# Kernel tuning notes

Hardware: AMD Instinct MI355X
Metric: run time of the kernel (lower is better)

## Reference

```python
import jax, jax.numpy as jnp
import numpy as np

N_NODES = 10000
N_EDGES = 640000
IN_DIM = 128
HID = 128
N_GRAPHS = 64


def setup_inputs() -> dict:
    key = jax.random.key(0)
    ks = jax.random.split(key, 9)
    x = jax.random.normal(ks[0], (N_NODES, IN_DIM), dtype=jnp.float32)
    edge_index = jax.random.randint(ks[1], (2, N_EDGES), 0, N_NODES, dtype=jnp.int32)
    batch = jnp.sort(jax.random.randint(ks[2], (N_NODES,), 0, N_GRAPHS, dtype=jnp.int32))
    # GCNConv weights (glorot-ish init) and zero biases
    W0 = jax.random.normal(ks[3], (IN_DIM, HID), dtype=jnp.float32) / np.float32(np.sqrt(IN_DIM))
    b0 = jnp.zeros((HID,), dtype=jnp.float32)
    W1 = jax.random.normal(ks[4], (HID, HID), dtype=jnp.float32) / np.float32(np.sqrt(HID))
    b1 = jnp.zeros((HID,), dtype=jnp.float32)
    W2 = jax.random.normal(ks[5], (HID, HID), dtype=jnp.float32) / np.float32(np.sqrt(HID))
    b2 = jnp.zeros((HID,), dtype=jnp.float32)
    return {"x": x, "edge_index": edge_index, "batch": batch,
            "W0": W0, "b0": b0, "W1": W1, "b1": b1, "W2": W2, "b2": b2}


def _gcn_conv(x, src, dst, W, b, n_nodes):
    """PyG GCNConv: self-loops + symmetric normalization, then linear+bias."""
    h = x @ W  # [N, H]
    # degree of destination nodes, +1 for the added self-loop
    deg = jax.ops.segment_sum(jnp.ones((src.shape[0],), h.dtype), dst,
                              num_segments=n_nodes) + 1.0
    dis = jax.lax.rsqrt(deg)  # deg >= 1 so no inf guard needed
    # messages along real edges, normalized by dis[src]*dis[dst]
    msg = h[src] * (dis[src] * dis[dst])[:, None]  # [E, H]
    out = jax.ops.segment_sum(msg, dst, num_segments=n_nodes)
    # self-loop contribution: dis[i]^2 * h[i]
    out = out + h * (dis * dis)[:, None]
    return out + b


def reference(x, edge_index, batch, W0, b0, W1, b1, W2, b2):
    src, dst = edge_index[0], edge_index[1]
    n_nodes = x.shape[0]
    # layer 0 and 1 followed by ReLU (dropout: eval mode -> identity)
    h = _gcn_conv(x, src, dst, W0, b0, n_nodes)
    h = jax.nn.relu(h)
    h = _gcn_conv(h, src, dst, W1, b1, n_nodes)
    h = jax.nn.relu(h)
    h = _gcn_conv(h, src, dst, W2, b2, n_nodes)
    # global mean pool over batch indices
    sums = jax.ops.segment_sum(h, batch, num_segments=N_GRAPHS)  # [B, H]
    counts = jax.ops.segment_sum(jnp.ones((n_nodes,), h.dtype), batch,
                                 num_segments=N_GRAPHS)
    return sums / jnp.maximum(counts, 1.0)[:, None]
```

## Files before the change

kernel.cpp:

```cpp
#include <hip/hip_runtime.h>
#include <hip/hip_fp16.h>

#define NN 10000
#define NE 640000
#define NG 64
#define CAP 128
#define NB 625
#define BCAP 1280

typedef _Float16 f16x8 __attribute__((ext_vector_type(8)));
typedef float f32x4 __attribute__((ext_vector_type(4)));

__device__ __forceinline__ void split8v(float4 xa, float4 xb, f16x8& ah, f16x8& al) {
    float x[8] = {xa.x, xa.y, xa.z, xa.w, xb.x, xb.y, xb.z, xb.w};
#pragma unroll
    for (int j = 0; j < 8; j++) {
        ah[j] = (_Float16)x[j];
        al[j] = (_Float16)(x[j] - (float)ah[j]);
    }
}

__global__ __launch_bounds__(256) void k_initp1(
    const int* __restrict__ batch, int* __restrict__ gstart,
    const float* __restrict__ W0, const float* __restrict__ W1, const float* __restrict__ W2,
    __half* __restrict__ wh, __half* __restrict__ wl,
    const int* __restrict__ ei, int* __restrict__ bcur, int* __restrict__ pk,
    __half* __restrict__ g16a, __half* __restrict__ g16b)
{
    __shared__ int hist[NB];
    int bid = blockIdx.x, t = threadIdx.x;
    if (bid < 40) {
        int i = bid * 256 + t;
        if (i < NN) {
            int b = batch[i];
            int prev = (i == 0) ? -1 : batch[i - 1];
            for (int g = prev + 1; g <= b; g++) gstart[g] = i;
            if (i == NN - 1)
                for (int g = b + 1; g <= NG; g++) gstart[g] = NN;
        }
    } else if (bid < 232) {
        int wid = bid - 40;
        int z = wid >> 6;
        int q = (wid & 63) * 256 + t;
        int c = q >> 7, k = q & 127;
        const float* W = (z == 0) ? W0 : (z == 1) ? W1 : W2;
        float v = W[k * 128 + c];
        __half h = __float2half(v);
        __half lo = __float2half(v - __half2float(h));
        wh[z * 16384 + c * 128 + k] = h;
        wl[z * 16384 + c * 128 + k] = lo;
    } else if (bid < 389) {
        for (int q = t; q < NB; q += 256) hist[q] = 0;
        __syncthreads();
        int4 s4[4], d4[4];
        int ebase = (bid - 232) * 4096;
#pragma unroll
        for (int q = 0; q < 4; q++) {
            int e = ebase + q * 1024 + t * 4;
            if (e < NE) {
                s4[q] = *(const int4*)&ei[e];
                d4[q] = *(const int4*)&ei[NE + e];
                atomicAdd(&hist[d4[q].x >> 4], 1);
                atomicAdd(&hist[d4[q].y >> 4], 1);
                atomicAdd(&hist[d4[q].z >> 4], 1);
                atomicAdd(&hist[d4[q].w >> 4], 1);
            }
        }
        __syncthreads();
        for (int q = t; q < NB; q += 256) {
            int h = hist[q];
            hist[q] = (h > 0) ? atomicAdd(&bcur[q], h) : 0;
        }
        __syncthreads();
#pragma unroll
        for (int q = 0; q < 4; q++) {
            int e = ebase + q * 1024 + t * 4;
            if (e < NE) {
                int b0i = d4[q].x >> 4, b1i = d4[q].y >> 4, b2i = d4[q].z >> 4, b3i = d4[q].w >> 4;
                int r0 = atomicAdd(&hist[b0i], 1);
                int r1 = atomicAdd(&hist[b1i], 1);
                int r2 = atomicAdd(&hist[b2i], 1);
                int r3 = atomicAdd(&hist[b3i], 1);
                if (r0 < BCAP) pk[b0i * BCAP + r0] = s4[q].x | ((d4[q].x & 15) << 14);
                if (r1 < BCAP) pk[b1i * BCAP + r1] = s4[q].y | ((d4[q].y & 15) << 14);
                if (r2 < BCAP) pk[b2i * BCAP + r2] = s4[q].z | ((d4[q].z & 15) << 14);
                if (r3 < BCAP) pk[b3i * BCAP + r3] = s4[q].w | ((d4[q].w & 15) << 14);
            }
        }
    } else {
        uint4 z = {0u, 0u, 0u, 0u};
        ((uint4*)(g16a + NN * 128))[t] = z;
        ((uint4*)(g16b + NN * 128))[t] = z;
    }
}

__global__ __launch_bounds__(512) void k_p2g0(
    const int* __restrict__ bcur, const int* __restrict__ pk,
    const float* __restrict__ x,
    const __half* __restrict__ whT, const __half* __restrict__ wlT,
    int* __restrict__ deg, int* __restrict__ csrc, __half* __restrict__ g16a)
{
    __shared__ int buf[16 * CAP];
    __shared__ int cnt[16];
    int b = blockIdx.x, t = threadIdx.x;
    if (t < 16) cnt[t] = 0;
    __syncthreads();

    int n = bcur[b];
    if (n > BCAP) n = BCAP;
    const int* pb = &pk[b * BCAP];
    for (int i = t; i < n; i += 512) {
        int v = pb[i];
        int nd = v >> 14;
        int slot = atomicAdd(&cnt[nd], 1);
        if (slot < CAP) buf[(nd << 7) + slot] = v & 0x3FFF;
    }
    __syncthreads();

    int node0 = b << 4;
    if (t < 16) {
        int c = cnt[t];
        deg[node0 + t] = c;
        buf[(t << 7) + min(c, CAP - 1)] = NN;
    }
    __syncthreads();

    ((int4*)&csrc[node0 << 7])[t] = ((const int4*)buf)[t];

    int w = t >> 6, l = t & 63, lr = l & 15, lg = l >> 4;
    int cw = w * 16;
    const _Float16* whp = (const _Float16*)whT;
    const _Float16* wlp = (const _Float16*)wlT;
    f32x4 acc = {0.f, 0.f, 0.f, 0.f};
#pragma unroll
    for (int ks = 0; ks < 4; ks++) {
        int kb = ks * 32 + lg * 8;
        f16x8 ah, al;
        split8v(*(const float4*)&x[(node0 + lr) * 128 + kb],
                *(const float4*)&x[(node0 + lr) * 128 + kb + 4], ah, al);
        int c0 = cw + lr;
        f16x8 bh = *(const f16x8*)&whp[c0 * 128 + kb];
        f16x8 bl = *(const f16x8*)&wlp[c0 * 128 + kb];
        acc = __builtin_amdgcn_mfma_f32_16x16x32_f16(ah, bh, acc, 0, 0, 0);
        acc = __builtin_amdgcn_mfma_f32_16x16x32_f16(al, bh, acc, 0, 0, 0);
        acc = __builtin_amdgcn_mfma_f32_16x16x32_f16(ah, bl, acc, 0, 0, 0);
    }
#pragma unroll
    for (int reg = 0; reg < 4; reg++) {
        int row = lg * 4 + reg;
        float d = rsqrtf((float)cnt[row] + 1.0f);
        g16a[(node0 + row) * 128 + cw + lr] = __float2half(acc[reg] * d);
    }
}

__device__ __forceinline__ void accp(uint2 v, float2& p, float2& q) {
    float2 f0 = __half22float2(*(__half2*)&v.x);
    float2 f1 = __half22float2(*(__half2*)&v.y);
    p.x += f0.x; p.y += f0.y; q.x += f1.x; q.y += f1.y;
}

__global__ __launch_bounds__(512) void k_ag(
    const __half* __restrict__ gin, const float* __restrict__ bias,
    const int* __restrict__ deg, const int* __restrict__ csrc,
    const __half* __restrict__ whT, const __half* __restrict__ wlT,
    __half* __restrict__ gout)
{
    __shared__ float Xs[16][132];
    int base = blockIdx.x << 4;
    int t = threadIdx.x;
    int w = t >> 6, l = t & 63;
    int half = l >> 5, li = l & 31;
    int co = li * 4;
#pragma unroll
    for (int k4 = 0; k4 < 2; k4++) {
        int row = w * 2 + k4;
        int i = base + row;
        int dgi = __builtin_amdgcn_readfirstlane(deg[i]);
        int nn_ = min(dgi, CAP - 1);
        int np = (nn_ + 1) & ~1;
        float2 A0 = {0.f, 0.f}, A1 = {0.f, 0.f};
        float2 B0 = {0.f, 0.f}, B1 = {0.f, 0.f};
        if (half == 0) {
            uint2 sv = *(const uint2*)&gin[i * 128 + co];
            A0 = __half22float2(*(__half2*)&sv.x);
            A1 = __half22float2(*(__half2*)&sv.y);
        }
        const int* cp = &csrc[i << 7];
        for (int bs = 0; bs < np; bs += 64) {
            int m = np - bs;
            if (m > 64) m = 64;
            int myedge = (l < m) ? cp[bs + l] : NN;
            int pairs = m >> 1;
            int j = 0;
            for (; j + 8 <= pairs; j += 8) {
                int r0 = __shfl(myedge, 2 * j + half);
                int r1 = __shfl(myedge, 2 * j + 2 + half);
                int r2 = __shfl(myedge, 2 * j + 4 + half);
                int r3 = __shfl(myedge, 2 * j + 6 + half);
                int r4 = __shfl(myedge, 2 * j + 8 + half);
                int r5 = __shfl(myedge, 2 * j + 10 + half);
                int r6 = __shfl(myedge, 2 * j + 12 + half);
                int r7 = __shfl(myedge, 2 * j + 14 + half);
                uint2 v0 = *(const uint2*)&gin[r0 * 128 + co];
                uint2 v1 = *(const uint2*)&gin[r1 * 128 + co];
                uint2 v2 = *(const uint2*)&gin[r2 * 128 + co];
                uint2 v3 = *(const uint2*)&gin[r3 * 128 + co];
                uint2 v4 = *(const uint2*)&gin[r4 * 128 + co];
                uint2 v5 = *(const uint2*)&gin[r5 * 128 + co];
                uint2 v6 = *(const uint2*)&gin[r6 * 128 + co];
                uint2 v7 = *(const uint2*)&gin[r7 * 128 + co];
                accp(v0, A0, A1); accp(v1, B0, B1);
                accp(v2, A0, A1); accp(v3, B0, B1);
                accp(v4, A0, A1); accp(v5, B0, B1);
                accp(v6, A0, A1); accp(v7, B0, B1);
            }
            for (; j < pairs; j++) {
                int r = __shfl(myedge, 2 * j + half);
                uint2 v = *(const uint2*)&gin[r * 128 + co];
                accp(v, A0, A1);
            }
        }
        A0.x += B0.x; A0.y += B0.y; A1.x += B1.x; A1.y += B1.y;
        A0.x += __shfl_xor(A0.x, 32);
        A0.y += __shfl_xor(A0.y, 32);
        A1.x += __shfl_xor(A1.x, 32);
        A1.y += __shfl_xor(A1.y, 32);
        if (half == 0) {
            float di = rsqrtf((float)dgi + 1.0f);
            float4 bb = *(const float4*)&bias[co];
            float4 o;
            o.x = fmaxf(di * A0.x + bb.x, 0.f);
            o.y = fmaxf(di * A0.y + bb.y, 0.f);
            o.z = fmaxf(di * A1.x + bb.z, 0.f);
            o.w = fmaxf(di * A1.y + bb.w, 0.f);
            *(float4*)&Xs[row][co] = o;
        }
    }
    __syncthreads();

    int lr = l & 15, lg = l >> 4;
    int cw = w * 16;
    const _Float16* whp = (const _Float16*)whT;
    const _Float16* wlp = (const _Float16*)wlT;
    f32x4 acc = {0.f, 0.f, 0.f, 0.f};
#pragma unroll
    for (int ks = 0; ks < 4; ks++) {
        int kb = ks * 32 + lg * 8;
        f16x8 ah, al;
        split8v(*(const float4*)&Xs[lr][kb], *(const float4*)&Xs[lr][kb + 4], ah, al);
        int c0 = cw + lr;
        f16x8 bh = *(const f16x8*)&whp[c0 * 128 + kb];
        f16x8 bl = *(const f16x8*)&wlp[c0 * 128 + kb];
        acc = __builtin_amdgcn_mfma_f32_16x16x32_f16(ah, bh, acc, 0, 0, 0);
        acc = __builtin_amdgcn_mfma_f32_16x16x32_f16(al, bh, acc, 0, 0, 0);
        acc = __builtin_amdgcn_mfma_f32_16x16x32_f16(ah, bl, acc, 0, 0, 0);
    }
#pragma unroll
    for (int reg = 0; reg < 4; reg++) {
        int row = lg * 4 + reg;
        float d = rsqrtf((float)deg[base + row] + 1.0f);
        gout[(base + row) * 128 + cw + lr] = __float2half(acc[reg] * d);
    }
}

__global__ __launch_bounds__(256) void k_agg(const __half* __restrict__ g16,
                                             const float* __restrict__ bias,
                                             const int* __restrict__ deg,
                                             const int* __restrict__ csrc,
                                             float* __restrict__ out) {
    int wid = blockIdx.x * 4 + (threadIdx.x >> 6);
    int l = threadIdx.x & 63;
    if (wid >= NN) return;
    int i = wid;
    int dgi = __builtin_amdgcn_readfirstlane(deg[i]);
    int n = min(dgi, CAP - 1);
    int np = (n + 1) & ~1;
    int half = l >> 5, li = l & 31;
    int co = li * 4;
    float2 A0 = {0.f, 0.f}, A1 = {0.f, 0.f};
    float2 B0 = {0.f, 0.f}, B1 = {0.f, 0.f};
    if (half == 0) {
        uint2 sv = *(const uint2*)&g16[i * 128 + co];
        A0 = __half22float2(*(__half2*)&sv.x);
        A1 = __half22float2(*(__half2*)&sv.y);
    }
    const int* cp = &csrc[i << 7];
    for (int base = 0; base < np; base += 64) {
        int m = np - base;
        if (m > 64) m = 64;
        int myedge = (l < m) ? cp[base + l] : NN;
        int pairs = m >> 1;
        int j = 0;
        for (; j + 8 <= pairs; j += 8) {
            int r0 = __shfl(myedge, 2 * j + half);
            int r1 = __shfl(myedge, 2 * j + 2 + half);
            int r2 = __shfl(myedge, 2 * j + 4 + half);
            int r3 = __shfl(myedge, 2 * j + 6 + half);
            int r4 = __shfl(myedge, 2 * j + 8 + half);
            int r5 = __shfl(myedge, 2 * j + 10 + half);
            int r6 = __shfl(myedge, 2 * j + 12 + half);
            int r7 = __shfl(myedge, 2 * j + 14 + half);
            uint2 v0 = *(const uint2*)&g16[r0 * 128 + co];
            uint2 v1 = *(const uint2*)&g16[r1 * 128 + co];
            uint2 v2 = *(const uint2*)&g16[r2 * 128 + co];
            uint2 v3 = *(const uint2*)&g16[r3 * 128 + co];
            uint2 v4 = *(const uint2*)&g16[r4 * 128 + co];
            uint2 v5 = *(const uint2*)&g16[r5 * 128 + co];
            uint2 v6 = *(const uint2*)&g16[r6 * 128 + co];
            uint2 v7 = *(const uint2*)&g16[r7 * 128 + co];
            accp(v0, A0, A1); accp(v1, B0, B1);
            accp(v2, A0, A1); accp(v3, B0, B1);
            accp(v4, A0, A1); accp(v5, B0, B1);
            accp(v6, A0, A1); accp(v7, B0, B1);
        }
        for (; j < pairs; j++) {
            int r = __shfl(myedge, 2 * j + half);
            uint2 v = *(const uint2*)&g16[r * 128 + co];
            accp(v, A0, A1);
        }
    }
    A0.x += B0.x; A0.y += B0.y; A1.x += B1.x; A1.y += B1.y;
    A0.x += __shfl_xor(A0.x, 32);
    A0.y += __shfl_xor(A0.y, 32);
    A1.x += __shfl_xor(A1.x, 32);
    A1.y += __shfl_xor(A1.y, 32);
    if (half == 0) {
        float di = rsqrtf((float)dgi + 1.0f);
        float4 bb = *(const float4*)&bias[co];
        float4 o;
        o.x = di * A0.x + bb.x;
        o.y = di * A0.y + bb.y;
        o.z = di * A1.x + bb.z;
        o.w = di * A1.y + bb.w;
        *(float4*)&out[i * 128 + co] = o;
    }
}

__global__ __launch_bounds__(256) void k_pool(const float* __restrict__ h,
                                              const int* __restrict__ gstart,
                                              float* __restrict__ out) {
    int g = blockIdx.x;
    int s = gstart[g], e = gstart[g + 1];
    int t = threadIdx.x;
    int c = t & 127, half = t >> 7;
    float acc = 0.f;
    for (int n = s + half; n < e; n += 2) acc += h[n * 128 + c];
    __shared__ float sm[256];
    sm[t] = acc;
    __syncthreads();
    if (half == 0) {
        float cnt = (float)max(e - s, 1);
        out[g * 128 + c] = (sm[c] + sm[128 + c]) / cnt;
    }
}

extern "C" void kernel_launch(void* const* d_in, const int* in_sizes, int n_in,
                              void* d_out, int out_size, void* d_ws, size_t ws_size,
                              hipStream_t stream) {
    const float* x     = (const float*)d_in[0];
    const int*   ei    = (const int*)d_in[1];
    const int*   batch = (const int*)d_in[2];
    const float* W0 = (const float*)d_in[3];
    const float* b0 = (const float*)d_in[4];
    const float* W1 = (const float*)d_in[5];
    const float* b1 = (const float*)d_in[6];
    const float* W2 = (const float*)d_in[7];
    const float* b2 = (const float*)d_in[8];
    float* out = (float*)d_out;

    float* ws    = (float*)d_ws;
    int*   deg   = (int*)ws;
    int*   gstart= (int*)(ws + 10240);
    int*   bcur  = (int*)(ws + 10320);
    int*   csrc  = (int*)(ws + 10960);
    __half* g16a = (__half*)(ws + 1290960);
    __half* g16b = (__half*)(ws + 1931984);
    float* abuf  = ws + 2573008;
    int*   pk    = (int*)(ws + 2573008);
    __half* wh   = (__half*)(ws + 3853008);
    __half* wlo  = (__half*)(ws + 3877584);

    hipMemsetAsync(bcur, 0, 640 * sizeof(int), stream);
    k_initp1<<<390, 256, 0, stream>>>(batch, gstart, W0, W1, W2, wh, wlo, ei, bcur, pk,
                                      g16a, g16b);
    k_p2g0<<<NB, 512, 0, stream>>>(bcur, pk, x, wh, wlo, deg, csrc, g16a);
    k_ag<<<NB, 512, 0, stream>>>(g16a, b0, deg, csrc, wh + 16384, wlo + 16384, g16b);
    k_ag<<<NB, 512, 0, stream>>>(g16b, b1, deg, csrc, wh + 32768, wlo + 32768, g16a);
    k_agg<<<2500, 256, 0, stream>>>(g16a, b2, deg, csrc, abuf);
    k_pool<<<NG, 256, 0, stream>>>(abuf, gstart, out);
}
```

Baseline: 184.7 us.

## Fuse final aggregation with mean pooling via atomics and last-block finalize

Merges the last GCN aggregation kernel with the global mean pool. Each node's output row is atomically added into per-graph sums, and the last block to finish (tracked by a ticket counter) divides by the node counts and writes the result. This drops a kernel launch and the write and re-read of the full node feature buffer. In exchange it adds many float atomics to 64 contended graph rows, a threadfence per block, and order-dependent float sums. The workspace layout is also reshuffled to zero the counters and sums in a single memset.

```diff
diff --git a/kernel.cpp b/kernel.cpp
--- a/kernel.cpp
+++ b/kernel.cpp
@@ -263,14 +263,17 @@
     }
 }
 
-__global__ __launch_bounds__(256) void k_agg(const __half* __restrict__ g16,
-                                             const float* __restrict__ bias,
-                                             const int* __restrict__ deg,
-                                             const int* __restrict__ csrc,
-                                             float* __restrict__ out) {
+__global__ __launch_bounds__(256) void k_aggpool(const __half* __restrict__ g16,
+                                                 const float* __restrict__ bias,
+                                                 const int* __restrict__ deg,
+                                                 const int* __restrict__ csrc,
+                                                 const int* __restrict__ batch,
+                                                 const int* __restrict__ gstart,
+                                                 float* __restrict__ psum,
+                                                 int* __restrict__ done,
+                                                 float* __restrict__ out) {
     int wid = blockIdx.x * 4 + (threadIdx.x >> 6);
     int l = threadIdx.x & 63;
-    if (wid >= NN) return;
     int i = wid;
     int dgi = __builtin_amdgcn_readfirstlane(deg[i]);
     int n = min(dgi, CAP - 1);
@@ -327,30 +330,27 @@
     if (half == 0) {
         float di = rsqrtf((float)dgi + 1.0f);
         float4 bb = *(const float4*)&bias[co];
-        float4 o;
-        o.x = di * A0.x + bb.x;
-        o.y = di * A0.y + bb.y;
-        o.z = di * A1.x + bb.z;
-        o.w = di * A1.y + bb.w;
-        *(float4*)&out[i * 128 + co] = o;
-    }
-}
-
-__global__ __launch_bounds__(256) void k_pool(const float* __restrict__ h,
-                                              const int* __restrict__ gstart,
-                                              float* __restrict__ out) {
-    int g = blockIdx.x;
-    int s = gstart[g], e = gstart[g + 1];
-    int t = threadIdx.x;
-    int c = t & 127, half = t >> 7;
-    float acc = 0.f;
-    for (int n = s + half; n < e; n += 2) acc += h[n * 128 + c];
-    __shared__ float sm[256];
-    sm[t] = acc;
-    __syncthreads();
-    if (half == 0) {
-        float cnt = (float)max(e - s, 1);
-        out[g * 128 + c] = (sm[c] + sm[128 + c]) / cnt;
+        int g = batch[i];
+        float* ps = &psum[g * 128 + co];
+        atomicAdd(&ps[0], di * A0.x + bb.x);
+        atomicAdd(&ps[1], di * A0.y + bb.y);
+        atomicAdd(&ps[2], di * A1.x + bb.z);
+        atomicAdd(&ps[3], di * A1.y + bb.w);
+    }
+    __threadfence();
+    __syncthreads();
+    __shared__ int ticket;
+    if (threadIdx.x == 0) ticket = atomicAdd(done, 1);
+    __syncthreads();
+    if (ticket == 2499) {
+        __threadfence();
+        int t = threadIdx.x;
+        for (int q = t; q < NG * 128; q += 256) {
+            int g = q >> 7;
+            float cnt = (float)max(gstart[g + 1] - gstart[g], 1);
+            float v = __hip_atomic_load(&psum[q], __ATOMIC_RELAXED, __HIP_MEMORY_SCOPE_AGENT);
+            out[q] = v / cnt;
+        }
     }
 }
 
@@ -372,20 +372,20 @@
     int*   deg   = (int*)ws;
     int*   gstart= (int*)(ws + 10240);
     int*   bcur  = (int*)(ws + 10320);
-    int*   csrc  = (int*)(ws + 10960);
-    __half* g16a = (__half*)(ws + 1290960);
-    __half* g16b = (__half*)(ws + 1931984);
-    float* abuf  = ws + 2573008;
-    int*   pk    = (int*)(ws + 2573008);
-    __half* wh   = (__half*)(ws + 3853008);
-    __half* wlo  = (__half*)(ws + 3877584);
-
-    hipMemsetAsync(bcur, 0, 640 * sizeof(int), stream);
+    int*   done  = (int*)(ws + 10960);
+    float* psum  = ws + 10976;
+    int*   csrc  = (int*)(ws + 19168);
+    __half* g16a = (__half*)(ws + 1299168);
+    __half* g16b = (__half*)(ws + 1940192);
+    int*   pk    = (int*)(ws + 2581216);
+    __half* wh   = (__half*)(ws + 3381216);
+    __half* wlo  = (__half*)(ws + 3405792);
+
+    hipMemsetAsync(ws + 10320, 0, (640 + 16 + 8192) * sizeof(int), stream);
     k_initp1<<<390, 256, 0, stream>>>(batch, gstart, W0, W1, W2, wh, wlo, ei, bcur, pk,
                                       g16a, g16b);
     k_p2g0<<<NB, 512, 0, stream>>>(bcur, pk, x, wh, wlo, deg, csrc, g16a);
     k_ag<<<NB, 512, 0, stream>>>(g16a, b0, deg, csrc, wh + 16384, wlo + 16384, g16b);
     k_ag<<<NB, 512, 0, stream>>>(g16b, b1, deg, csrc, wh + 32768, wlo + 32768, g16a);
-    k_agg<<<2500, 256, 0, stream>>>(g16a, b2, deg, csrc, abuf);
-    k_pool<<<NG, 256, 0, stream>>>(abuf, gstart, out);
-}
+    k_aggpool<<<2500, 256, 0, stream>>>(g16a, b2, deg, csrc, batch, gstart, psum, done, out);
+}
```

After: 332.6 us. 1.8x slower.

## Fuse final aggregation with mean pooling via atomic adds into output

Applied to the files above, without the earlier changes.

The last-layer aggregation now scales each node's result by its graph's inverse count and atomically adds it into the pooled output, removing the intermediate [N,128] float buffer and the separate pool kernel. The output is pre-initialized with bias (or zero for empty graphs) by block 0 of an earlier kernel. This saves one launch and a full write/read of the node features, but adds many float atomics contending on only 64 graph rows, and the summation order becomes nondeterministic.

```diff
diff --git a/kernel.cpp b/kernel.cpp
--- a/kernel.cpp
+++ b/kernel.cpp
@@ -98,11 +98,19 @@
     const int* __restrict__ bcur, const int* __restrict__ pk,
     const float* __restrict__ x,
     const __half* __restrict__ whT, const __half* __restrict__ wlT,
-    int* __restrict__ deg, int* __restrict__ csrc, __half* __restrict__ g16a)
+    const float* __restrict__ b2, const int* __restrict__ gstart,
+    int* __restrict__ deg, int* __restrict__ csrc, __half* __restrict__ g16a,
+    float* __restrict__ out)
 {
     __shared__ int buf[16 * CAP];
     __shared__ int cnt[16];
     int b = blockIdx.x, t = threadIdx.x;
+    if (b == 0) {
+        for (int q = t; q < NG * 128; q += 512) {
+            int g = q >> 7;
+            out[q] = (gstart[g + 1] > gstart[g]) ? b2[q & 127] : 0.f;
+        }
+    }
     if (t < 16) cnt[t] = 0;
     __syncthreads();
 
@@ -263,14 +271,14 @@
     }
 }
 
-__global__ __launch_bounds__(256) void k_agg(const __half* __restrict__ g16,
-                                             const float* __restrict__ bias,
-                                             const int* __restrict__ deg,
-                                             const int* __restrict__ csrc,
-                                             float* __restrict__ out) {
+__global__ __launch_bounds__(256) void k_aggpool(const __half* __restrict__ g16,
+                                                 const int* __restrict__ deg,
+                                                 const int* __restrict__ csrc,
+                                                 const int* __restrict__ batch,
+                                                 const int* __restrict__ gstart,
+                                                 float* __restrict__ out) {
     int wid = blockIdx.x * 4 + (threadIdx.x >> 6);
     int l = threadIdx.x & 63;
-    if (wid >= NN) return;
     int i = wid;
     int dgi = __builtin_amdgcn_readfirstlane(deg[i]);
     int n = min(dgi, CAP - 1);
@@ -326,31 +334,14 @@
     A1.y += __shfl_xor(A1.y, 32);
     if (half == 0) {
         float di = rsqrtf((float)dgi + 1.0f);
-        float4 bb = *(const float4*)&bias[co];
-        float4 o;
-        o.x = di * A0.x + bb.x;
-        o.y = di * A0.y + bb.y;
-        o.z = di * A1.x + bb.z;
-        o.w = di * A1.y + bb.w;
-        *(float4*)&out[i * 128 + co] = o;
-    }
-}
-
-__global__ __launch_bounds__(256) void k_pool(const float* __restrict__ h,
-                                              const int* __restrict__ gstart,
-                                              float* __restrict__ out) {
-    int g = blockIdx.x;
-    int s = gstart[g], e = gstart[g + 1];
-    int t = threadIdx.x;
-    int c = t & 127, half = t >> 7;
-    float acc = 0.f;
-    for (int n = s + half; n < e; n += 2) acc += h[n * 128 + c];
-    __shared__ float sm[256];
-    sm[t] = acc;
-    __syncthreads();
-    if (half == 0) {
-        float cnt = (float)max(e - s, 1);
-        out[g * 128 + c] = (sm[c] + sm[128 + c]) / cnt;
+        int g = batch[i];
+        float icnt = 1.0f / (float)max(gstart[g + 1] - gstart[g], 1);
+        float s = di * icnt;
+        float* op = &out[g * 128 + co];
+        atomicAdd(&op[0], s * A0.x);
+        atomicAdd(&op[1], s * A0.y);
+        atomicAdd(&op[2], s * A1.x);
+        atomicAdd(&op[3], s * A1.y);
     }
 }
 
@@ -375,17 +366,15 @@
     int*   csrc  = (int*)(ws + 10960);
     __half* g16a = (__half*)(ws + 1290960);
     __half* g16b = (__half*)(ws + 1931984);
-    float* abuf  = ws + 2573008;
     int*   pk    = (int*)(ws + 2573008);
-    __half* wh   = (__half*)(ws + 3853008);
-    __half* wlo  = (__half*)(ws + 3877584);
+    __half* wh   = (__half*)(ws + 3373008);
+    __half* wlo  = (__half*)(ws + 3397584);
 
     hipMemsetAsync(bcur, 0, 640 * sizeof(int), stream);
     k_initp1<<<390, 256, 0, stream>>>(batch, gstart, W0, W1, W2, wh, wlo, ei, bcur, pk,
                                       g16a, g16b);
-    k_p2g0<<<NB, 512, 0, stream>>>(bcur, pk, x, wh, wlo, deg, csrc, g16a);
+    k_p2g0<<<NB, 512, 0, stream>>>(bcur, pk, x, wh, wlo, b2, gstart, deg, csrc, g16a, out);
     k_ag<<<NB, 512, 0, stream>>>(g16a, b0, deg, csrc, wh + 16384, wlo + 16384, g16b);
     k_ag<<<NB, 512, 0, stream>>>(g16b, b1, deg, csrc, wh + 32768, wlo + 32768, g16a);
-    k_agg<<<2500, 256, 0, stream>>>(g16a, b2, deg, csrc, abuf);
-    k_pool<<<NG, 256, 0, stream>>>(abuf, gstart, out);
-}
+    k_aggpool<<<2500, 256, 0, stream>>>(g16a, deg, csrc, batch, gstart, out);
+}
```

Result: slower. 203.4 us (+10.1%).
